# Kernel tuning notes

Hardware: AMD Instinct MI355X
Metric: run time of the kernel (lower is better)

## Reference

```python
import jax, jax.numpy as jnp
import numpy as np
import math

B, S, H = 4, 2048, 1024
NH, HD = 16, 64
BASE = 10000.0

def _rope_cos_sin(seq_len, dim):
    inv_freq = 1.0 / (BASE ** (jnp.arange(0, dim, 2, dtype=jnp.float32) / dim))
    pos = jnp.arange(seq_len, dtype=jnp.float32)
    freqs = jnp.outer(pos, inv_freq)              # [S, dim/2]
    emb = jnp.concatenate([freqs, freqs], axis=-1)  # [S, dim]
    return jnp.cos(emb), jnp.sin(emb)

def _apply_rotary(x, cos, sin):
    # x: [B, NH, S, HD]; cos/sin: [S, HD]
    d = x.shape[-1] // 2
    x1, x2 = x[..., :d], x[..., d:]
    rotated = jnp.concatenate([-x2, x1], axis=-1)
    return x * cos[None, None] + rotated * sin[None, None]

def setup_inputs() -> dict:
    key = jax.random.key(0)
    ks = jax.random.split(key, 5)
    scale = 1.0 / math.sqrt(H)
    return {
        "x": jax.random.normal(ks[0], (B, S, H), dtype=jnp.float32),
        "attention_mask": jnp.ones((B, S), dtype=jnp.int32),
        "Wq": jax.random.normal(ks[1], (H, H), dtype=jnp.float32) * scale,
        "Wk": jax.random.normal(ks[2], (H, H), dtype=jnp.float32) * scale,
        "Wv": jax.random.normal(ks[3], (H, H), dtype=jnp.float32) * scale,
        "Wo": jax.random.normal(ks[4], (H, H), dtype=jnp.float32) * scale,
    }

def reference(x, attention_mask, Wq, Wk, Wv, Wo):
    b, s, _ = x.shape
    # projections (nn.Linear: x @ W.T)
    q = (x @ Wq.T).reshape(b, s, NH, HD).transpose(0, 2, 1, 3)  # [B,NH,S,HD]
    k = (x @ Wk.T).reshape(b, s, NH, HD).transpose(0, 2, 1, 3)
    v = (x @ Wv.T).reshape(b, s, NH, HD).transpose(0, 2, 1, 3)
    cos, sin = _rope_cos_sin(s, HD)
    q = _apply_rotary(q, cos, sin)
    k = _apply_rotary(k, cos, sin)
    scores = jnp.einsum('bhqd,bhkd->bhqk', q, k) / math.sqrt(HD)
    mask = attention_mask[:, None, None, :]  # [B,1,1,S]
    scores = jnp.where(mask == 0, -jnp.inf, scores)
    attn = jax.nn.softmax(scores, axis=-1)
    out = jnp.einsum('bhqk,bhkd->bhqd', attn, v)
    out = out.transpose(0, 2, 1, 3).reshape(b, s, NH * HD)
    return out @ Wo.T
```

## Files before the change

kernel.cpp:

```cpp
#include <hip/hip_runtime.h>
#include <hip/hip_bf16.h>

#define B_  4
#define S_  2048
#define H_  1024
#define NH_ 16
#define HD_ 64

typedef __bf16 bf16;
typedef __attribute__((ext_vector_type(8))) __bf16 bf16x8;
typedef __attribute__((ext_vector_type(4))) __bf16 bf16x4;
typedef __attribute__((ext_vector_type(4))) float f32x4;

typedef const __attribute__((address_space(1))) char* gptr_t;
typedef __attribute__((address_space(3))) char* lptr_t;
#define GLOAD_LDS16(g, l) __builtin_amdgcn_global_load_lds((gptr_t)(g), (lptr_t)(l), 16, 0, 0)

__device__ __forceinline__ f32x4 mfma16(bf16x8 a, bf16x8 b, f32x4 c) {
    return __builtin_amdgcn_mfma_f32_16x16x32_bf16(a, b, c, 0, 0, 0);
}

__device__ __forceinline__ void swz_bid(int& bx, int& by) {
    const int gx = gridDim.x;
    const int nwg = gx * gridDim.y;
    const int i = blockIdx.x + gx * blockIdx.y;
    const int w = (i & 7) * (nwg >> 3) + (i >> 3);
    bx = w % gx;
    by = w / gx;
}

__global__ void k_cvt(const float* __restrict__ src, bf16* __restrict__ dst, int n4) {
    int i = blockIdx.x * blockDim.x + threadIdx.x;
    if (i < n4) {
        float4 v = ((const float4*)src)[i];
        bf16x4 o;
        o[0] = (__bf16)v.x; o[1] = (__bf16)v.y; o[2] = (__bf16)v.z; o[3] = (__bf16)v.w;
        *(bf16x4*)(dst + i * 4) = o;
    }
}

__global__ void k_tab(float* __restrict__ cosT, float* __restrict__ sinT) {
    int i = blockIdx.x * blockDim.x + threadIdx.x;
    if (i >= S_ * 32) return;
    int s = i >> 5, d = i & 31;
    float inv = powf(10000.0f, -(float)d * (1.0f / 32.0f));
    float ang = (float)s * inv;
    cosT[i] = cosf(ang);
    sinT[i] = sinf(ang);
}

template<int EPI>
__global__ __launch_bounds__(256) void k_gemm(
        const bf16* __restrict__ A, const bf16* __restrict__ Bw,
        bf16* __restrict__ q_out, bf16* __restrict__ k_out, bf16* __restrict__ v_out,
        const float* __restrict__ cosT, const float* __restrict__ sinT,
        float* __restrict__ fout) {
    __shared__ bf16 As[128 * 32];
    __shared__ bf16 Bs[128 * 32];
    const int t = threadIdx.x, l = t & 63, w = t >> 6;
    const int lr = l & 15, hi = l >> 4;
    int bx, by;
    swz_bid(bx, by);
    const int m0 = by * 128, n0 = bx * 128;
    const int wr = (w >> 1) * 64, wc = (w & 1) * 64;
    f32x4 acc[4][4] = {};

    for (int k0 = 0; k0 < 1024; k0 += 32) {
        __syncthreads();
#pragma unroll
        for (int i = 0; i < 2; ++i) {
            int o = i * 4096 + t * 16;
            int row = o >> 6, colb = o & 63;
            GLOAD_LDS16((const char*)A + ((size_t)(m0 + row) * 1024 + k0) * 2 + colb,
                        (char*)As + o);
            GLOAD_LDS16((const char*)Bw + ((size_t)(n0 + row) * 1024 + k0) * 2 + colb,
                        (char*)Bs + o);
        }
        __syncthreads();
        bf16x8 af[4], bfr[4];
#pragma unroll
        for (int mi = 0; mi < 4; ++mi)
            af[mi] = *(const bf16x8*)&As[(wr + mi * 16 + lr) * 32 + hi * 8];
#pragma unroll
        for (int ni = 0; ni < 4; ++ni)
            bfr[ni] = *(const bf16x8*)&Bs[(wc + ni * 16 + lr) * 32 + hi * 8];
#pragma unroll
        for (int mi = 0; mi < 4; ++mi)
#pragma unroll
            for (int ni = 0; ni < 4; ++ni)
                acc[mi][ni] = mfma16(af[mi], bfr[ni], acc[mi][ni]);
    }

    if (EPI == 0) {
        const int nbase = n0 + wc;
        const int which = nbase >> 10;
        const int head = (nbase & 1023) >> 6;
        if (which == 2) {
#pragma unroll
            for (int mi = 0; mi < 4; ++mi) {
                int m = m0 + wr + mi * 16 + hi * 4;
                int bb = m >> 11, s = m & 2047;
                int st = s & 63;
                int pos = ((st >> 5) & 1) * 32 + ((st >> 2) & 3) * 8 + ((st >> 4) & 1) * 4;
                int sp = (s & ~63) | pos;
                size_t vbase = (size_t)(bb * NH_ + head) * HD_;
#pragma unroll
                for (int ni = 0; ni < 4; ++ni) {
                    bf16x4 o;
#pragma unroll
                    for (int r = 0; r < 4; ++r) o[r] = (__bf16)acc[mi][ni][r];
                    *(bf16x4*)(v_out + (vbase + ni * 16 + lr) * (size_t)S_ + sp) = o;
                }
            }
        } else {
            bf16* dst = which == 0 ? q_out : k_out;
            const float qsc = which == 0 ? 0.125f : 1.0f;
#pragma unroll
            for (int mi = 0; mi < 4; ++mi) {
#pragma unroll
                for (int r = 0; r < 4; ++r) {
                    int m = m0 + wr + mi * 16 + hi * 4 + r;
                    int bb = m >> 11, s = m & 2047;
                    size_t base = (((size_t)bb * NH_ + head) * S_ + s) * HD_;
#pragma unroll
                    for (int ni = 0; ni < 2; ++ni) {
                        int d = ni * 16 + lr;
                        float c = cosT[s * 32 + d] * qsc, sn = sinT[s * 32 + d] * qsc;
                        float x1 = acc[mi][ni][r], x2 = acc[mi][ni + 2][r];
                        dst[base + d]      = (__bf16)(x1 * c - x2 * sn);
                        dst[base + d + 32] = (__bf16)(x2 * c + x1 * sn);
                    }
                }
            }
        }
    } else {
#pragma unroll
        for (int mi = 0; mi < 4; ++mi)
#pragma unroll
            for (int ni = 0; ni < 4; ++ni)
#pragma unroll
                for (int r = 0; r < 4; ++r)
                    fout[(size_t)(m0 + wr + mi * 16 + hi * 4 + r) * 1024
                         + (n0 + wc + ni * 16 + lr)] = acc[mi][ni][r];
    }
}

__global__ __launch_bounds__(256, 3) void k_attn(
        const bf16* __restrict__ qr, const bf16* __restrict__ kr,
        const bf16* __restrict__ vt, const int* __restrict__ mask,
        bf16* __restrict__ aout) {
    __shared__ bf16 Ks[2][64 * 64];
    __shared__ bf16 Vs[2][64 * 64];
    const int t = threadIdx.x, l = t & 63, w = t >> 6;
    const int lr = l & 15, hi = l >> 4;
    const int sw = (lr & 7) << 4;
    int bx, by;
    swz_bid(bx, by);
    const int bh = by, b = bh >> 4, head = bh & 15;
    const int qbase = bx * 128 + w * 32;

    const bf16* Qb = qr + (size_t)bh * S_ * HD_;
    const char* Kg = (const char*)(kr + (size_t)bh * S_ * HD_);
    const char* Vg = (const char*)(vt + (size_t)bh * HD_ * S_);
    const int* mrow = mask + b * S_;

    bf16x8 qf[2][2];
#pragma unroll
    for (int qh = 0; qh < 2; ++qh)
#pragma unroll
        for (int h = 0; h < 2; ++h)
            qf[qh][h] = *(const bf16x8*)(Qb + (size_t)(qbase + qh * 16 + lr) * HD_ + h * 32 + hi * 8);

    int anyz0 = 0;
    for (int i = l; i < S_ / 4; i += 64) {
        int4 m4 = ((const int4*)mrow)[i];
        anyz0 |= (m4.x == 0) | (m4.y == 0) | (m4.z == 0) | (m4.w == 0);
    }
    const bool anyz = __any(anyz0);

    f32x4 acc[4][2] = {};
    float mrun[2] = {-1e30f, -1e30f};
    float lrun[2] = {0.0f, 0.0f};

    auto STAGE = [&](int buf, int kv0) {
#pragma unroll
        for (int i = 0; i < 2; ++i) {
            int o = i * 4096 + t * 16;
            int row = o >> 7, colb = o & 127;
            int scol = colb ^ ((row & 7) << 4);
            GLOAD_LDS16(Kg + (size_t)(kv0 + row) * 128 + scol, (char*)Ks[buf] + o);
            GLOAD_LDS16(Vg + (size_t)row * (S_ * 2) + (size_t)kv0 * 2 + scol,
                        (char*)Vs[buf] + o);
        }
    };

    STAGE(0, 0);
    const int NT = S_ / 64;
    for (int ti = 0; ti < NT; ++ti) {
        __syncthreads();
        if (ti + 1 < NT) STAGE((ti + 1) & 1, (ti + 1) * 64);
        const char* Kc = (const char*)Ks[ti & 1];
        const char* Vc = (const char*)Vs[ti & 1];
        const int kv0 = ti * 64;

        f32x4 st[4][2] = {};
#pragma unroll
        for (int g = 0; g < 4; ++g) {
            int rb = (g * 16 + lr) * 128;
            bf16x8 kf0 = *(const bf16x8*)(Kc + rb + ((hi * 16) ^ sw));
            bf16x8 kf1 = *(const bf16x8*)(Kc + rb + ((64 + hi * 16) ^ sw));
            st[g][0] = mfma16(kf0, qf[0][0], st[g][0]);
            st[g][0] = mfma16(kf1, qf[0][1], st[g][0]);
            st[g][1] = mfma16(kf0, qf[1][0], st[g][1]);
            st[g][1] = mfma16(kf1, qf[1][1], st[g][1]);
        }

        if (anyz) {
#pragma unroll
            for (int g = 0; g < 4; ++g) {
                int4 mv = *(const int4*)(mrow + kv0 + g * 16 + hi * 4);
#pragma unroll
                for (int qh = 0; qh < 2; ++qh) {
                    st[g][qh][0] = mv.x ? st[g][qh][0] : -INFINITY;
                    st[g][qh][1] = mv.y ? st[g][qh][1] : -INFINITY;
                    st[g][qh][2] = mv.z ? st[g][qh][2] : -INFINITY;
                    st[g][qh][3] = mv.w ? st[g][qh][3] : -INFINITY;
                }
            }
        }

        float tm[2];
#pragma unroll
        for (int qh = 0; qh < 2; ++qh) {
            float m_ = st[0][qh][0];
#pragma unroll
            for (int g = 0; g < 4; ++g)
#pragma unroll
                for (int r = 0; r < 4; ++r) m_ = fmaxf(m_, st[g][qh][r]);
            m_ = fmaxf(m_, __shfl_xor(m_, 16));
            m_ = fmaxf(m_, __shfl_xor(m_, 32));
            tm[qh] = m_;
        }

        bool need = (tm[0] > mrun[0] + 8.0f) || (tm[1] > mrun[1] + 8.0f);
        if (__any(need)) {
#pragma unroll
            for (int qh = 0; qh < 2; ++qh) {
                float mn = fmaxf(mrun[qh], tm[qh]);
                float corr = __expf(mrun[qh] - mn);
                lrun[qh] *= corr;
#pragma unroll
                for (int dt = 0; dt < 4; ++dt) acc[dt][qh] *= corr;
                mrun[qh] = mn;
            }
        }

        bf16x8 pB[2][2];
#pragma unroll
        for (int qh = 0; qh < 2; ++qh) {
            float ts = 0.0f;
#pragma unroll
            for (int g = 0; g < 4; ++g)
#pragma unroll
                for (int r = 0; r < 4; ++r) {
                    float e = __expf(st[g][qh][r] - mrun[qh]);
                    pB[qh][g >> 1][(g & 1) * 4 + r] = (__bf16)e;
                    ts += e;
                }
            ts += __shfl_xor(ts, 16);
            ts += __shfl_xor(ts, 32);
            lrun[qh] += ts;
        }

#pragma unroll
        for (int dt = 0; dt < 4; ++dt) {
            const char* vrow = Vc + (dt * 16 + lr) * 128;
#pragma unroll
            for (int ks = 0; ks < 2; ++ks) {
                bf16x8 vf = *(const bf16x8*)(vrow + ((ks * 64 + hi * 16) ^ sw));
                acc[dt][0] = mfma16(vf, pB[0][ks], acc[dt][0]);
                acc[dt][1] = mfma16(vf, pB[1][ks], acc[dt][1]);
            }
        }
    }

    float inv[2] = {1.0f / lrun[0], 1.0f / lrun[1]};
#pragma unroll
    for (int qh = 0; qh < 2; ++qh) {
        size_t obase = ((size_t)(b * S_ + qbase + qh * 16 + lr)) * H_ + head * HD_;
#pragma unroll
        for (int dt = 0; dt < 4; ++dt) {
            bf16x4 o;
#pragma unroll
            for (int r = 0; r < 4; ++r) o[r] = (__bf16)(acc[dt][qh][r] * inv[qh]);
            *(bf16x4*)(aout + obase + dt * 16 + hi * 4) = o;
        }
    }
}

extern "C" void kernel_launch(void* const* d_in, const int* in_sizes, int n_in,
                              void* d_out, int out_size, void* d_ws, size_t ws_size,
                              hipStream_t stream) {
    const float* x  = (const float*)d_in[0];
    const int* mask = (const int*)d_in[1];
    const float* Wq = (const float*)d_in[2];
    const float* Wk = (const float*)d_in[3];
    const float* Wv = (const float*)d_in[4];
    const float* Wo = (const float*)d_in[5];
    float* out = (float*)d_out;

    char* ws = (char*)d_ws;
    bf16* xb    = (bf16*)ws;
    bf16* wqkv  = (bf16*)(ws + (size_t)16 * 1048576);
    bf16* wob   = (bf16*)(ws + (size_t)22 * 1048576);
    bf16* qr    = (bf16*)(ws + (size_t)24 * 1048576);
    bf16* kr    = (bf16*)(ws + (size_t)40 * 1048576);
    bf16* vtw   = (bf16*)(ws + (size_t)56 * 1048576);
    float* cosT = (float*)(ws + (size_t)72 * 1048576);
    float* sinT = (float*)(ws + (size_t)72 * 1048576 + 262144);

    k_cvt<<<2097152 / 256, 256, 0, stream>>>(x, xb, 2097152);
    k_cvt<<<262144 / 256, 256, 0, stream>>>(Wq, wqkv, 262144);
    k_cvt<<<262144 / 256, 256, 0, stream>>>(Wk, wqkv + 1048576, 262144);
    k_cvt<<<262144 / 256, 256, 0, stream>>>(Wv, wqkv + 2097152, 262144);
    k_cvt<<<262144 / 256, 256, 0, stream>>>(Wo, wob, 262144);
    k_tab<<<256, 256, 0, stream>>>(cosT, sinT);

    k_gemm<0><<<dim3(24, 64), 256, 0, stream>>>(xb, wqkv, qr, kr, vtw, cosT, sinT, nullptr);

    k_attn<<<dim3(16, 64), 256, 0, stream>>>(qr, kr, vtw, mask, xb);

    k_gemm<1><<<dim3(8, 64), 256, 0, stream>>>(xb, wob, nullptr, nullptr, nullptr,
                                               nullptr, nullptr, out);
}
```

Baseline: 235.8 us.

## Use exp2 softmax, MFMA row sums, 512-thread attention blocks, and MFMA priority

Folds log2(e) into the Q scale so the softmax can use exp2 directly. Row-sum accumulation moves from shuffles to MFMA against a ones vector, which removes the cross-lane reductions. Attention blocks grow to 8 waves covering 256 queries, so each K/V tile staged in LDS is shared by twice as many waves. The change also adds s_setprio around the MFMA sections, a tree-shaped max reduction, and a higher rescale threshold. The risks are bf16-rounded probabilities entering the denominator and a looser rescale bound.

```diff
diff --git a/kernel.cpp b/kernel.cpp
--- a/kernel.cpp
+++ b/kernel.cpp
@@ -114,7 +114,7 @@
             }
         } else {
             bf16* dst = which == 0 ? q_out : k_out;
-            const float qsc = which == 0 ? 0.125f : 1.0f;
+            const float qsc = which == 0 ? 0.125f * 1.4426950408889634f : 1.0f;
 #pragma unroll
             for (int mi = 0; mi < 4; ++mi) {
 #pragma unroll
@@ -145,7 +145,7 @@
     }
 }
 
-__global__ __launch_bounds__(256, 3) void k_attn(
+__global__ __launch_bounds__(512, 4) void k_attn(
         const bf16* __restrict__ qr, const bf16* __restrict__ kr,
         const bf16* __restrict__ vt, const int* __restrict__ mask,
         bf16* __restrict__ aout) {
@@ -157,7 +157,7 @@
     int bx, by;
     swz_bid(bx, by);
     const int bh = by, b = bh >> 4, head = bh & 15;
-    const int qbase = bx * 128 + w * 32;
+    const int qbase = bx * 256 + w * 32;
 
     const bf16* Qb = qr + (size_t)bh * S_ * HD_;
     const char* Kg = (const char*)(kr + (size_t)bh * S_ * HD_);
@@ -171,6 +171,10 @@
         for (int h = 0; h < 2; ++h)
             qf[qh][h] = *(const bf16x8*)(Qb + (size_t)(qbase + qh * 16 + lr) * HD_ + h * 32 + hi * 8);
 
+    bf16x8 onesf;
+#pragma unroll
+    for (int j = 0; j < 8; ++j) onesf[j] = (__bf16)1.0f;
+
     int anyz0 = 0;
     for (int i = l; i < S_ / 4; i += 64) {
         int4 m4 = ((const int4*)mrow)[i];
@@ -179,19 +183,16 @@
     const bool anyz = __any(anyz0);
 
     f32x4 acc[4][2] = {};
+    f32x4 accL[2] = {};
     float mrun[2] = {-1e30f, -1e30f};
-    float lrun[2] = {0.0f, 0.0f};
 
     auto STAGE = [&](int buf, int kv0) {
-#pragma unroll
-        for (int i = 0; i < 2; ++i) {
-            int o = i * 4096 + t * 16;
-            int row = o >> 7, colb = o & 127;
-            int scol = colb ^ ((row & 7) << 4);
-            GLOAD_LDS16(Kg + (size_t)(kv0 + row) * 128 + scol, (char*)Ks[buf] + o);
-            GLOAD_LDS16(Vg + (size_t)row * (S_ * 2) + (size_t)kv0 * 2 + scol,
-                        (char*)Vs[buf] + o);
-        }
+        int o = t * 16;
+        int row = o >> 7, colb = o & 127;
+        int scol = colb ^ ((row & 7) << 4);
+        GLOAD_LDS16(Kg + (size_t)(kv0 + row) * 128 + scol, (char*)Ks[buf] + o);
+        GLOAD_LDS16(Vg + (size_t)row * (S_ * 2) + (size_t)kv0 * 2 + scol,
+                    (char*)Vs[buf] + o);
     };
 
     STAGE(0, 0);
@@ -204,6 +205,7 @@
         const int kv0 = ti * 64;
 
         f32x4 st[4][2] = {};
+        __builtin_amdgcn_s_setprio(1);
 #pragma unroll
         for (int g = 0; g < 4; ++g) {
             int rb = (g * 16 + lr) * 128;
@@ -214,6 +216,7 @@
             st[g][1] = mfma16(kf0, qf[1][0], st[g][1]);
             st[g][1] = mfma16(kf1, qf[1][1], st[g][1]);
         }
+        __builtin_amdgcn_s_setprio(0);
 
         if (anyz) {
 #pragma unroll
@@ -232,23 +235,26 @@
         float tm[2];
 #pragma unroll
         for (int qh = 0; qh < 2; ++qh) {
-            float m_ = st[0][qh][0];
-#pragma unroll
-            for (int g = 0; g < 4; ++g)
-#pragma unroll
-                for (int r = 0; r < 4; ++r) m_ = fmaxf(m_, st[g][qh][r]);
+            float r8[8];
+#pragma unroll
+            for (int j = 0; j < 8; ++j)
+                r8[j] = fmaxf(st[j >> 2][qh][j & 3], st[2 + (j >> 2)][qh][j & 3]);
+            float r4[4];
+#pragma unroll
+            for (int j = 0; j < 4; ++j) r4[j] = fmaxf(r8[j], r8[j + 4]);
+            float m_ = fmaxf(fmaxf(r4[0], r4[1]), fmaxf(r4[2], r4[3]));
             m_ = fmaxf(m_, __shfl_xor(m_, 16));
             m_ = fmaxf(m_, __shfl_xor(m_, 32));
             tm[qh] = m_;
         }
 
-        bool need = (tm[0] > mrun[0] + 8.0f) || (tm[1] > mrun[1] + 8.0f);
+        bool need = (tm[0] > mrun[0] + 11.5f) || (tm[1] > mrun[1] + 11.5f);
         if (__any(need)) {
 #pragma unroll
             for (int qh = 0; qh < 2; ++qh) {
                 float mn = fmaxf(mrun[qh], tm[qh]);
-                float corr = __expf(mrun[qh] - mn);
-                lrun[qh] *= corr;
+                float corr = __builtin_exp2f(mrun[qh] - mn);
+                accL[qh][0] *= corr;
 #pragma unroll
                 for (int dt = 0; dt < 4; ++dt) acc[dt][qh] *= corr;
                 mrun[qh] = mn;
@@ -257,21 +263,19 @@
 
         bf16x8 pB[2][2];
 #pragma unroll
-        for (int qh = 0; qh < 2; ++qh) {
-            float ts = 0.0f;
+        for (int qh = 0; qh < 2; ++qh)
 #pragma unroll
             for (int g = 0; g < 4; ++g)
 #pragma unroll
-                for (int r = 0; r < 4; ++r) {
-                    float e = __expf(st[g][qh][r] - mrun[qh]);
-                    pB[qh][g >> 1][(g & 1) * 4 + r] = (__bf16)e;
-                    ts += e;
-                }
-            ts += __shfl_xor(ts, 16);
-            ts += __shfl_xor(ts, 32);
-            lrun[qh] += ts;
-        }
-
+                for (int r = 0; r < 4; ++r)
+                    pB[qh][g >> 1][(g & 1) * 4 + r] =
+                        (__bf16)__builtin_exp2f(st[g][qh][r] - mrun[qh]);
+
+        __builtin_amdgcn_s_setprio(1);
+        accL[0] = mfma16(onesf, pB[0][0], accL[0]);
+        accL[0] = mfma16(onesf, pB[0][1], accL[0]);
+        accL[1] = mfma16(onesf, pB[1][0], accL[1]);
+        accL[1] = mfma16(onesf, pB[1][1], accL[1]);
 #pragma unroll
         for (int dt = 0; dt < 4; ++dt) {
             const char* vrow = Vc + (dt * 16 + lr) * 128;
@@ -282,9 +286,10 @@
                 acc[dt][1] = mfma16(vf, pB[1][ks], acc[dt][1]);
             }
         }
-    }
-
-    float inv[2] = {1.0f / lrun[0], 1.0f / lrun[1]};
+        __builtin_amdgcn_s_setprio(0);
+    }
+
+    float inv[2] = {1.0f / accL[0][0], 1.0f / accL[1][0]};
 #pragma unroll
     for (int qh = 0; qh < 2; ++qh) {
         size_t obase = ((size_t)(b * S_ + qbase + qh * 16 + lr)) * H_ + head * HD_;
@@ -328,7 +333,7 @@
 
     k_gemm<0><<<dim3(24, 64), 256, 0, stream>>>(xb, wqkv, qr, kr, vtw, cosT, sinT, nullptr);
 
-    k_attn<<<dim3(16, 64), 256, 0, stream>>>(qr, kr, vtw, mask, xb);
+    k_attn<<<dim3(8, 64), 512, 0, stream>>>(qr, kr, vtw, mask, xb);
 
     k_gemm<1><<<dim3(8, 64), 256, 0, stream>>>(xb, wob, nullptr, nullptr, nullptr,
                                                nullptr, nullptr, out);
```

After: 241.1 us. 2.2% more time.
